# Performance work log

Hardware: AMD Instinct MI355X
Metric: run time of the kernel (lower is better)

The kernel has to match this reference:

```python
import jax, jax.numpy as jnp
import numpy as np

NT = 128
T = 262144


def setup_inputs() -> dict:
    key = jax.random.key(0)
    k1, k2, k3, k4, k5 = jax.random.split(key, 5)
    emit = jax.random.normal(k1, (T, NT), dtype=jnp.float32)
    y = jax.random.randint(k2, (T,), 0, NT, dtype=jnp.int64)
    trans = jax.random.normal(k3, (NT, NT), dtype=jnp.float32)
    strans = jax.random.normal(k4, (NT,), dtype=jnp.float32)
    etrans = jax.random.normal(k5, (NT,), dtype=jnp.float32)
    return {"emit": emit, "y": y, "trans": trans, "strans": strans, "etrans": etrans}


def _crf_nll(emit, y, trans, strans, etrans):
    Tlen = emit.shape[0]

    # forward algorithm (log partition) via scan over timesteps 1..T-1
    alpha0 = strans + emit[0]  # [nt]

    def step(alpha, e_t):
        # alpha_new[n] = logsumexp_p(alpha[p] + trans[p, n]) + emit_t[n]
        alpha_new = jax.nn.logsumexp(alpha[:, None] + trans, axis=0) + e_t
        return alpha_new, None

    alpha, _ = jax.lax.scan(step, alpha0, emit[1:])
    logZ = jax.nn.logsumexp(alpha + etrans)

    # gold score (faithful to original: emissions indexed by the *previous* tag)
    prev = y[:-1]
    nxt = y[1:]
    score = strans[y[0]]
    score = score + jnp.sum(trans[prev, nxt] + emit[jnp.arange(Tlen - 1), prev])
    score = score + etrans[y[-1]] + emit[-1, y[-1]]

    return logZ - score


def reference(emit, y, trans, strans, etrans):
    return _crf_nll(emit, y, trans, strans, etrans)
```

## Files before the change

### kernel.cpp

```cpp
#include <hip/hip_runtime.h>

typedef float f32x4 __attribute__((ext_vector_type(4)));

#define T_LEN   262144
#define NTAG    128
#define LCH     8
#define BURN    8
#define NSTEP   (LCH + BURN)
#define NCHUNK  (T_LEN / LCH)
#define NWAVE   (NCHUNK / 16)
#define NFWDB   (NWAVE / 4)
#define NSCOREB 256
#define NBLK    (NFWDB + NSCOREB)

__global__ __launch_bounds__(256, 1) void crf_all(
    const float* __restrict__ emit, const int* __restrict__ y,
    const float* __restrict__ trans, const float* __restrict__ strans,
    const float* __restrict__ etrans, double* __restrict__ ws,
    float* __restrict__ out)
{
  if (blockIdx.x < NFWDB) {
    const int w   = threadIdx.x >> 6;
    const int l   = threadIdx.x & 63;
    const int col = l & 15;
    const int grp = l >> 4;
    const int gw  = blockIdx.x * 4 + w;
    const int gc  = gw * 16 + col;

    long a[8][4];
#pragma unroll
    for (int rt = 0; rt < 8; ++rt) {
      const int outtag = 16 * rt + col;
#pragma unroll
      for (int kt = 0; kt < 4; ++kt) {
        float q[8];
#pragma unroll
        for (int j = 0; j < 8; ++j) {
          const int k = 32 * kt + 4 * grp + (j & 3) + 16 * (j >> 2);
          q[j] = __expf(trans[k * NTAG + outtag]);
        }
        unsigned lo = (unsigned)__builtin_amdgcn_cvt_pk_fp8_f32(q[0], q[1], 0, false);
        lo = (unsigned)__builtin_amdgcn_cvt_pk_fp8_f32(q[2], q[3], (int)lo, true);
        unsigned hi = (unsigned)__builtin_amdgcn_cvt_pk_fp8_f32(q[4], q[5], 0, false);
        hi = (unsigned)__builtin_amdgcn_cvt_pk_fp8_f32(q[6], q[7], (int)hi, true);
        a[rt][kt] = (long)(((unsigned long long)hi << 32) | lo);
      }
    }

    float acc = 0.f;
    long b[4];
    {
      float u[8][4];
      if (gc == 0) {
        float vm = -1e30f;
#pragma unroll
        for (int rt = 0; rt < 8; ++rt)
#pragma unroll
          for (int r = 0; r < 4; ++r) {
            const int tag = 16 * rt + 4 * grp + r;
            u[rt][r] = strans[tag] + emit[tag];
            vm = fmaxf(vm, u[rt][r]);
          }
        vm = fmaxf(vm, __shfl_xor(vm, 16, 64));
        vm = fmaxf(vm, __shfl_xor(vm, 32, 64));
        acc = vm;
#pragma unroll
        for (int rt = 0; rt < 8; ++rt)
#pragma unroll
          for (int r = 0; r < 4; ++r) u[rt][r] = __expf(u[rt][r] - vm);
      } else {
#pragma unroll
        for (int rt = 0; rt < 8; ++rt)
#pragma unroll
          for (int r = 0; r < 4; ++r) u[rt][r] = 1.0f;
      }
#pragma unroll
      for (int kt = 0; kt < 4; ++kt) {
        unsigned lo = (unsigned)__builtin_amdgcn_cvt_pk_fp8_f32(u[2*kt][0], u[2*kt][1], 0, false);
        lo = (unsigned)__builtin_amdgcn_cvt_pk_fp8_f32(u[2*kt][2], u[2*kt][3], (int)lo, true);
        unsigned hi = (unsigned)__builtin_amdgcn_cvt_pk_fp8_f32(u[2*kt+1][0], u[2*kt+1][1], 0, false);
        hi = (unsigned)__builtin_amdgcn_cvt_pk_fp8_f32(u[2*kt+1][2], u[2*kt+1][3], (int)hi, true);
        b[kt] = (long)(((unsigned long long)hi << 32) | lo);
      }
    }

    const int t0 = (gc == 0) ? 1 : (gc * LCH - BURN);
    float4 pf[8];
    {
      const float* ep = emit + ((size_t)t0 << 7) + 4 * grp;
#pragma unroll
      for (int rt = 0; rt < 8; ++rt) pf[rt] = *(const float4*)(ep + 16 * rt);
    }

#pragma unroll 1
    for (int s = 0; s < NSTEP; ++s) {
      f32x4 c[8];
#pragma unroll
      for (int rt = 0; rt < 8; ++rt) c[rt] = (f32x4){0.f, 0.f, 0.f, 0.f};
#pragma unroll
      for (int kt = 0; kt < 4; ++kt)
#pragma unroll
        for (int rt = 0; rt < 8; ++rt)
          c[rt] = __builtin_amdgcn_mfma_f32_16x16x32_fp8_fp8(a[rt][kt], b[kt], c[rt], 0, 0, 0);

      float vm = -1e30f;
#pragma unroll
      for (int rt = 0; rt < 8; ++rt) {
        c[rt][0] *= __expf(pf[rt].x);
        c[rt][1] *= __expf(pf[rt].y);
        c[rt][2] *= __expf(pf[rt].z);
        c[rt][3] *= __expf(pf[rt].w);
        vm = fmaxf(vm, fmaxf(fmaxf(c[rt][0], c[rt][1]), fmaxf(c[rt][2], c[rt][3])));
      }
      if (s < NSTEP - 1) {
        const float* ep = emit + ((size_t)(t0 + s + 1) << 7) + 4 * grp;
#pragma unroll
        for (int rt = 0; rt < 8; ++rt) pf[rt] = *(const float4*)(ep + 16 * rt);
      }

      vm = fmaxf(vm, __shfl_xor(vm, 16, 64));
      vm = fmaxf(vm, __shfl_xor(vm, 32, 64));
      const bool on = (gc == 0) ? (s <= LCH - 2) : (s >= BURN);
      if (on) acc += __logf(vm);
      const float rinv = __frcp_rn(vm);
#pragma unroll
      for (int kt = 0; kt < 4; ++kt) {
        const float s0 = c[2*kt][0] * rinv,   s1 = c[2*kt][1] * rinv;
        const float s2 = c[2*kt][2] * rinv,   s3 = c[2*kt][3] * rinv;
        const float s4 = c[2*kt+1][0] * rinv, s5 = c[2*kt+1][1] * rinv;
        const float s6 = c[2*kt+1][2] * rinv, s7 = c[2*kt+1][3] * rinv;
        unsigned lo = (unsigned)__builtin_amdgcn_cvt_pk_fp8_f32(s0, s1, 0, false);
        lo = (unsigned)__builtin_amdgcn_cvt_pk_fp8_f32(s2, s3, (int)lo, true);
        unsigned hi = (unsigned)__builtin_amdgcn_cvt_pk_fp8_f32(s4, s5, 0, false);
        hi = (unsigned)__builtin_amdgcn_cvt_pk_fp8_f32(s6, s7, (int)hi, true);
        b[kt] = (long)(((unsigned long long)hi << 32) | lo);
      }

      if (s == NSTEP - 1 && gc == NCHUNK - 1) {
        float lv = 0.f;
#pragma unroll
        for (int rt = 0; rt < 8; ++rt)
#pragma unroll
          for (int r = 0; r < 4; ++r)
            lv += (c[rt][r] * rinv) * __expf(etrans[16 * rt + 4 * grp + r]);
        lv += __shfl_xor(lv, 16, 64);
        lv += __shfl_xor(lv, 32, 64);
        if (l == 15) atomicAdd(&ws[2], (double)lv);
      }
    }

    float av = (grp == 0) ? acc : 0.f;
#pragma unroll
    for (int off = 1; off < 64; off <<= 1) av += __shfl_xor(av, off, 64);
    if (l == 0) atomicAdd(&ws[0], (double)av);
  } else {
    __shared__ float sred[4];
    int idx0 = (blockIdx.x - NFWDB) * 256 + threadIdx.x;
    float v = 0.f;
    for (int t = idx0; t < T_LEN - 1; t += NSCOREB * 256) {
      int yt = y[t], yn = y[t + 1];
      v += trans[yt * NTAG + yn] + emit[(size_t)t * NTAG + yt];
    }
    if (idx0 == 0) {
      int yl = y[T_LEN - 1];
      v += strans[y[0]] + etrans[yl] + emit[(size_t)(T_LEN - 1) * NTAG + yl];
    }
#pragma unroll
    for (int off = 1; off < 64; off <<= 1) v += __shfl_xor(v, off, 64);
    if ((threadIdx.x & 63) == 0) sred[threadIdx.x >> 6] = v;
    __syncthreads();
    if (threadIdx.x == 0)
      atomicAdd(&ws[1], (double)(sred[0] + sred[1] + sred[2] + sred[3]));
  }

  __syncthreads();
  if (threadIdx.x == 0) {
    __threadfence();
    unsigned t = atomicAdd((unsigned*)&ws[3], 1u);
    if (t == NBLK - 1) {
      double d0 = atomicAdd(&ws[0], 0.0);
      double d1 = atomicAdd(&ws[1], 0.0);
      double d2 = atomicAdd(&ws[2], 0.0);
      out[0] = (float)(d0 + log(d2) - d1);
    }
  }
}

extern "C" void kernel_launch(void* const* d_in, const int* in_sizes, int n_in,
                              void* d_out, int out_size, void* d_ws, size_t ws_size,
                              hipStream_t stream)
{
  const float* emit   = (const float*)d_in[0];
  const int*   y      = (const int*)d_in[1];
  const float* trans  = (const float*)d_in[2];
  const float* strans = (const float*)d_in[3];
  const float* etrans = (const float*)d_in[4];
  float*  out = (float*)d_out;
  double* ws  = (double*)d_ws;

  hipMemsetAsync(ws, 0, 4 * sizeof(double), stream);
  crf_all<<<dim3(NBLK), dim3(256), 0, stream>>>(
      emit, y, trans, strans, etrans, ws, out);
}
```

Measured before the change: 92.53 us.

## Split CRF kernel, precompute fp8 transition matrix, renormalize every four steps

New measurement: 82.38 us. -11.0%, faster.

```diff
diff --git a/kernel.cpp b/kernel.cpp
--- a/kernel.cpp
+++ b/kernel.cpp
@@ -6,35 +6,26 @@
 #define NTAG    128
 #define LCH     8
 #define BURN    8
-#define NSTEP   (LCH + BURN)
+#define NSTEP   16
 #define NCHUNK  (T_LEN / LCH)
 #define NWAVE   (NCHUNK / 16)
 #define NFWDB   (NWAVE / 4)
 #define NSCOREB 256
-#define NBLK    (NFWDB + NSCOREB)
-
-__global__ __launch_bounds__(256, 1) void crf_all(
-    const float* __restrict__ emit, const int* __restrict__ y,
-    const float* __restrict__ trans, const float* __restrict__ strans,
-    const float* __restrict__ etrans, double* __restrict__ ws,
-    float* __restrict__ out)
-{
-  if (blockIdx.x < NFWDB) {
-    const int w   = threadIdx.x >> 6;
-    const int l   = threadIdx.x & 63;
-    const int col = l & 15;
-    const int grp = l >> 4;
-    const int gw  = blockIdx.x * 4 + w;
-    const int gc  = gw * 16 + col;
-
-    long a[8][4];
-#pragma unroll
-    for (int rt = 0; rt < 8; ++rt) {
-      const int outtag = 16 * rt + col;
-#pragma unroll
-      for (int kt = 0; kt < 4; ++kt) {
+#define C9      6.23832462503951f
+#define K63LN2  43.66827237527655f
+#define K72LN2  49.90659700060892f
+
+__global__ void crf_setup(const float* __restrict__ trans, uint4* __restrict__ q4)
+{
+  const int l = threadIdx.x;
+  const int col = l & 15, grp = l >> 4;
+  for (int rt = 0; rt < 8; ++rt) {
+    const int outtag = 16 * rt + col;
+    for (int kp = 0; kp < 2; ++kp) {
+      unsigned r[4];
+      for (int h = 0; h < 2; ++h) {
+        const int kt = kp * 2 + h;
         float q[8];
-#pragma unroll
         for (int j = 0; j < 8; ++j) {
           const int k = 32 * kt + 4 * grp + (j & 3) + 16 * (j >> 2);
           q[j] = __expf(trans[k * NTAG + outtag]);
@@ -43,147 +34,204 @@
         lo = (unsigned)__builtin_amdgcn_cvt_pk_fp8_f32(q[2], q[3], (int)lo, true);
         unsigned hi = (unsigned)__builtin_amdgcn_cvt_pk_fp8_f32(q[4], q[5], 0, false);
         hi = (unsigned)__builtin_amdgcn_cvt_pk_fp8_f32(q[6], q[7], (int)hi, true);
-        a[rt][kt] = (long)(((unsigned long long)hi << 32) | lo);
+        r[h * 2] = lo; r[h * 2 + 1] = hi;
       }
-    }
-
-    float acc = 0.f;
-    long b[4];
-    {
-      float u[8][4];
-      if (gc == 0) {
-        float vm = -1e30f;
+      q4[(rt * 2 + kp) * 64 + l] = make_uint4(r[0], r[1], r[2], r[3]);
+    }
+  }
+}
+
+__global__ __launch_bounds__(256, 2) void crf_fwd(
+    const float* __restrict__ emit, const float* __restrict__ strans,
+    const float* __restrict__ etrans, const uint4* __restrict__ q4,
+    double* __restrict__ ws)
+{
+  const int w_id = threadIdx.x >> 6;
+  const int l    = threadIdx.x & 63;
+  const int col  = l & 15;
+  const int grp  = l >> 4;
+  const int gw   = blockIdx.x * 4 + w_id;
+  const int gc   = gw * 16 + col;
+
+  long a[8][4];
+#pragma unroll
+  for (int rt = 0; rt < 8; ++rt)
+#pragma unroll
+    for (int kp = 0; kp < 2; ++kp) {
+      uint4 v = q4[(rt * 2 + kp) * 64 + l];
+      a[rt][2 * kp]     = (long)(((unsigned long long)v.y << 32) | v.x);
+      a[rt][2 * kp + 1] = (long)(((unsigned long long)v.w << 32) | v.z);
+    }
+
+  float m0 = 0.f;
+  long b[4];
+  {
+    float u[8][4];
+    if (gw == 0) {
+      float vm = -1e30f;
+#pragma unroll
+      for (int rt = 0; rt < 8; ++rt)
+#pragma unroll
+        for (int r = 0; r < 4; ++r) {
+          const int tag = 16 * rt + 4 * grp + r;
+          u[rt][r] = (col == 0) ? (strans[tag] + emit[tag]) : 0.f;
+          vm = fmaxf(vm, u[rt][r]);
+        }
+      vm = fmaxf(vm, __shfl_xor(vm, 16, 64));
+      vm = fmaxf(vm, __shfl_xor(vm, 32, 64));
+      m0 = vm;
+#pragma unroll
+      for (int rt = 0; rt < 8; ++rt)
+#pragma unroll
+        for (int r = 0; r < 4; ++r)
+          u[rt][r] = (col == 0) ? __expf(u[rt][r] - vm) : 1.0f;
+    } else {
+#pragma unroll
+      for (int rt = 0; rt < 8; ++rt)
+#pragma unroll
+        for (int r = 0; r < 4; ++r) u[rt][r] = 1.0f;
+    }
+#pragma unroll
+    for (int kt = 0; kt < 4; ++kt) {
+      unsigned lo = (unsigned)__builtin_amdgcn_cvt_pk_fp8_f32(u[2*kt][0], u[2*kt][1], 0, false);
+      lo = (unsigned)__builtin_amdgcn_cvt_pk_fp8_f32(u[2*kt][2], u[2*kt][3], (int)lo, true);
+      unsigned hi = (unsigned)__builtin_amdgcn_cvt_pk_fp8_f32(u[2*kt+1][0], u[2*kt+1][1], 0, false);
+      hi = (unsigned)__builtin_amdgcn_cvt_pk_fp8_f32(u[2*kt+1][2], u[2*kt+1][3], (int)hi, true);
+      b[kt] = (long)(((unsigned long long)hi << 32) | lo);
+    }
+  }
+
+  const int t0 = (gc == 0) ? 1 : (gc * LCH - BURN);
+  float4 pf[2][8];
+  {
+    const float* e0 = emit + ((size_t)t0 << 7) + 4 * grp;
+    const float* e1 = emit + ((size_t)(t0 + 1) << 7) + 4 * grp;
+#pragma unroll
+    for (int rt = 0; rt < 8; ++rt) {
+      pf[0][rt] = *(const float4*)(e0 + 16 * rt);
+      pf[1][rt] = *(const float4*)(e1 + 16 * rt);
+    }
+  }
+
+  float acc = 0.f;
+
+#pragma unroll
+  for (int s = 0; s < NSTEP; ++s) {
+    float e[8][4];
+#pragma unroll
+    for (int rt = 0; rt < 8; ++rt) {
+      e[rt][0] = __expf(pf[s & 1][rt].x - C9);
+      e[rt][1] = __expf(pf[s & 1][rt].y - C9);
+      e[rt][2] = __expf(pf[s & 1][rt].z - C9);
+      e[rt][3] = __expf(pf[s & 1][rt].w - C9);
+    }
+    if (s < NSTEP - 2) {
+      const float* ep = emit + ((size_t)(t0 + s + 2) << 7) + 4 * grp;
+#pragma unroll
+      for (int rt = 0; rt < 8; ++rt) pf[s & 1][rt] = *(const float4*)(ep + 16 * rt);
+    }
+
+    f32x4 c[8];
+#pragma unroll
+    for (int rt = 0; rt < 8; ++rt) c[rt] = (f32x4){0.f, 0.f, 0.f, 0.f};
+#pragma unroll
+    for (int kt = 0; kt < 4; ++kt)
+#pragma unroll
+      for (int rt = 0; rt < 8; ++rt)
+        c[rt] = __builtin_amdgcn_mfma_f32_16x16x32_fp8_fp8(a[rt][kt], b[kt], c[rt], 0, 0, 0);
+
+    float w[8][4];
+#pragma unroll
+    for (int rt = 0; rt < 8; ++rt)
+#pragma unroll
+      for (int r = 0; r < 4; ++r) w[rt][r] = c[rt][r] * e[rt][r];
+
+    if ((s & 3) == 3) {
+      float vm = w[0][0];
+#pragma unroll
+      for (int rt = 0; rt < 8; ++rt)
+#pragma unroll
+        for (int r = 0; r < 4; ++r) vm = fmaxf(vm, w[rt][r]);
+      vm = fmaxf(vm, __shfl_xor(vm, 16, 64));
+      vm = fmaxf(vm, __shfl_xor(vm, 32, 64));
+      const float lv = __logf(vm);
+      if (s == 3)  acc += (gc == 0) ? lv : 0.f;
+      if (s == 11) acc += (gc != 0) ? lv : 0.f;
+      if (s == 15) acc += (gc != 0) ? lv : 0.f;
+      const float rinv = __builtin_amdgcn_rcpf(vm);
+#pragma unroll
+      for (int rt = 0; rt < 8; ++rt)
+#pragma unroll
+        for (int r = 0; r < 4; ++r) w[rt][r] *= rinv;
+
+      if (s == NSTEP - 1 && gw == NWAVE - 1) {
+        float lse = 0.f;
 #pragma unroll
         for (int rt = 0; rt < 8; ++rt)
 #pragma unroll
-          for (int r = 0; r < 4; ++r) {
-            const int tag = 16 * rt + 4 * grp + r;
-            u[rt][r] = strans[tag] + emit[tag];
-            vm = fmaxf(vm, u[rt][r]);
-          }
+          for (int r = 0; r < 4; ++r)
+            lse += w[rt][r] * __expf(etrans[16 * rt + 4 * grp + r]);
+        lse += __shfl_xor(lse, 16, 64);
+        lse += __shfl_xor(lse, 32, 64);
+        if (l == 15) atomicAdd(&ws[2], (double)lse);
+      }
+    }
+    if (s == 6) {
+      if (gw == 0) {
+        float vm = w[0][0];
+#pragma unroll
+        for (int rt = 0; rt < 8; ++rt)
+#pragma unroll
+          for (int r = 0; r < 4; ++r) vm = fmaxf(vm, w[rt][r]);
         vm = fmaxf(vm, __shfl_xor(vm, 16, 64));
         vm = fmaxf(vm, __shfl_xor(vm, 32, 64));
-        acc = vm;
-#pragma unroll
-        for (int rt = 0; rt < 8; ++rt)
-#pragma unroll
-          for (int r = 0; r < 4; ++r) u[rt][r] = __expf(u[rt][r] - vm);
-      } else {
-#pragma unroll
-        for (int rt = 0; rt < 8; ++rt)
-#pragma unroll
-          for (int r = 0; r < 4; ++r) u[rt][r] = 1.0f;
+        acc += (gc == 0) ? __logf(vm) : 0.f;
       }
-#pragma unroll
-      for (int kt = 0; kt < 4; ++kt) {
-        unsigned lo = (unsigned)__builtin_amdgcn_cvt_pk_fp8_f32(u[2*kt][0], u[2*kt][1], 0, false);
-        lo = (unsigned)__builtin_amdgcn_cvt_pk_fp8_f32(u[2*kt][2], u[2*kt][3], (int)lo, true);
-        unsigned hi = (unsigned)__builtin_amdgcn_cvt_pk_fp8_f32(u[2*kt+1][0], u[2*kt+1][1], 0, false);
-        hi = (unsigned)__builtin_amdgcn_cvt_pk_fp8_f32(u[2*kt+1][2], u[2*kt+1][3], (int)hi, true);
-        b[kt] = (long)(((unsigned long long)hi << 32) | lo);
-      }
-    }
-
-    const int t0 = (gc == 0) ? 1 : (gc * LCH - BURN);
-    float4 pf[8];
-    {
-      const float* ep = emit + ((size_t)t0 << 7) + 4 * grp;
-#pragma unroll
-      for (int rt = 0; rt < 8; ++rt) pf[rt] = *(const float4*)(ep + 16 * rt);
-    }
-
-#pragma unroll 1
-    for (int s = 0; s < NSTEP; ++s) {
-      f32x4 c[8];
-#pragma unroll
-      for (int rt = 0; rt < 8; ++rt) c[rt] = (f32x4){0.f, 0.f, 0.f, 0.f};
-#pragma unroll
-      for (int kt = 0; kt < 4; ++kt)
-#pragma unroll
-        for (int rt = 0; rt < 8; ++rt)
-          c[rt] = __builtin_amdgcn_mfma_f32_16x16x32_fp8_fp8(a[rt][kt], b[kt], c[rt], 0, 0, 0);
-
-      float vm = -1e30f;
-#pragma unroll
-      for (int rt = 0; rt < 8; ++rt) {
-        c[rt][0] *= __expf(pf[rt].x);
-        c[rt][1] *= __expf(pf[rt].y);
-        c[rt][2] *= __expf(pf[rt].z);
-        c[rt][3] *= __expf(pf[rt].w);
-        vm = fmaxf(vm, fmaxf(fmaxf(c[rt][0], c[rt][1]), fmaxf(c[rt][2], c[rt][3])));
-      }
-      if (s < NSTEP - 1) {
-        const float* ep = emit + ((size_t)(t0 + s + 1) << 7) + 4 * grp;
-#pragma unroll
-        for (int rt = 0; rt < 8; ++rt) pf[rt] = *(const float4*)(ep + 16 * rt);
-      }
-
-      vm = fmaxf(vm, __shfl_xor(vm, 16, 64));
-      vm = fmaxf(vm, __shfl_xor(vm, 32, 64));
-      const bool on = (gc == 0) ? (s <= LCH - 2) : (s >= BURN);
-      if (on) acc += __logf(vm);
-      const float rinv = __frcp_rn(vm);
-#pragma unroll
-      for (int kt = 0; kt < 4; ++kt) {
-        const float s0 = c[2*kt][0] * rinv,   s1 = c[2*kt][1] * rinv;
-        const float s2 = c[2*kt][2] * rinv,   s3 = c[2*kt][3] * rinv;
-        const float s4 = c[2*kt+1][0] * rinv, s5 = c[2*kt+1][1] * rinv;
-        const float s6 = c[2*kt+1][2] * rinv, s7 = c[2*kt+1][3] * rinv;
-        unsigned lo = (unsigned)__builtin_amdgcn_cvt_pk_fp8_f32(s0, s1, 0, false);
-        lo = (unsigned)__builtin_amdgcn_cvt_pk_fp8_f32(s2, s3, (int)lo, true);
-        unsigned hi = (unsigned)__builtin_amdgcn_cvt_pk_fp8_f32(s4, s5, 0, false);
-        hi = (unsigned)__builtin_amdgcn_cvt_pk_fp8_f32(s6, s7, (int)hi, true);
-        b[kt] = (long)(((unsigned long long)hi << 32) | lo);
-      }
-
-      if (s == NSTEP - 1 && gc == NCHUNK - 1) {
-        float lv = 0.f;
-#pragma unroll
-        for (int rt = 0; rt < 8; ++rt)
-#pragma unroll
-          for (int r = 0; r < 4; ++r)
-            lv += (c[rt][r] * rinv) * __expf(etrans[16 * rt + 4 * grp + r]);
-        lv += __shfl_xor(lv, 16, 64);
-        lv += __shfl_xor(lv, 32, 64);
-        if (l == 15) atomicAdd(&ws[2], (double)lv);
-      }
-    }
-
-    float av = (grp == 0) ? acc : 0.f;
-#pragma unroll
-    for (int off = 1; off < 64; off <<= 1) av += __shfl_xor(av, off, 64);
-    if (l == 0) atomicAdd(&ws[0], (double)av);
-  } else {
-    __shared__ float sred[4];
-    int idx0 = (blockIdx.x - NFWDB) * 256 + threadIdx.x;
-    float v = 0.f;
-    for (int t = idx0; t < T_LEN - 1; t += NSCOREB * 256) {
-      int yt = y[t], yn = y[t + 1];
-      v += trans[yt * NTAG + yn] + emit[(size_t)t * NTAG + yt];
-    }
-    if (idx0 == 0) {
-      int yl = y[T_LEN - 1];
-      v += strans[y[0]] + etrans[yl] + emit[(size_t)(T_LEN - 1) * NTAG + yl];
-    }
-#pragma unroll
-    for (int off = 1; off < 64; off <<= 1) v += __shfl_xor(v, off, 64);
-    if ((threadIdx.x & 63) == 0) sred[threadIdx.x >> 6] = v;
-    __syncthreads();
-    if (threadIdx.x == 0)
-      atomicAdd(&ws[1], (double)(sred[0] + sred[1] + sred[2] + sred[3]));
-  }
-
+    }
+
+#pragma unroll
+    for (int kt = 0; kt < 4; ++kt) {
+      unsigned lo = (unsigned)__builtin_amdgcn_cvt_pk_fp8_f32(w[2*kt][0], w[2*kt][1], 0, false);
+      lo = (unsigned)__builtin_amdgcn_cvt_pk_fp8_f32(w[2*kt][2], w[2*kt][3], (int)lo, true);
+      unsigned hi = (unsigned)__builtin_amdgcn_cvt_pk_fp8_f32(w[2*kt+1][0], w[2*kt+1][1], 0, false);
+      hi = (unsigned)__builtin_amdgcn_cvt_pk_fp8_f32(w[2*kt+1][2], w[2*kt+1][3], (int)hi, true);
+      b[kt] = (long)(((unsigned long long)hi << 32) | lo);
+    }
+  }
+
+  const float accf = acc + ((gc == 0) ? (m0 + K63LN2) : K72LN2);
+  float av = (grp == 0) ? accf : 0.f;
+#pragma unroll
+  for (int off = 1; off < 64; off <<= 1) av += __shfl_xor(av, off, 64);
+  if (l == 0) atomicAdd(&ws[0], (double)av);
+}
+
+__global__ void crf_score(const float* __restrict__ emit, const int* __restrict__ y,
+                          const float* __restrict__ trans, const float* __restrict__ strans,
+                          const float* __restrict__ etrans, double* __restrict__ ws)
+{
+  __shared__ float sred[4];
+  int idx0 = blockIdx.x * 256 + threadIdx.x;
+  float v = 0.f;
+  for (int t = idx0; t < T_LEN - 1; t += NSCOREB * 256) {
+    int yt = y[t], yn = y[t + 1];
+    v += trans[yt * NTAG + yn] + emit[(size_t)t * NTAG + yt];
+  }
+  if (idx0 == 0) {
+    int yl = y[T_LEN - 1];
+    v += strans[y[0]] + etrans[yl] + emit[(size_t)(T_LEN - 1) * NTAG + yl];
+  }
+#pragma unroll
+  for (int off = 1; off < 64; off <<= 1) v += __shfl_xor(v, off, 64);
+  if ((threadIdx.x & 63) == 0) sred[threadIdx.x >> 6] = v;
   __syncthreads();
-  if (threadIdx.x == 0) {
-    __threadfence();
-    unsigned t = atomicAdd((unsigned*)&ws[3], 1u);
-    if (t == NBLK - 1) {
-      double d0 = atomicAdd(&ws[0], 0.0);
-      double d1 = atomicAdd(&ws[1], 0.0);
-      double d2 = atomicAdd(&ws[2], 0.0);
-      out[0] = (float)(d0 + log(d2) - d1);
-    }
-  }
+  if (threadIdx.x == 0)
+    atomicAdd(&ws[1], (double)(sred[0] + sred[1] + sred[2] + sred[3]));
+}
+
+__global__ void crf_final(const double* __restrict__ ws, float* __restrict__ out)
+{
+  out[0] = (float)(ws[0] + log(ws[2]) - ws[1]);
 }
 
 extern "C" void kernel_launch(void* const* d_in, const int* in_sizes, int n_in,
@@ -197,8 +245,11 @@
   const float* etrans = (const float*)d_in[4];
   float*  out = (float*)d_out;
   double* ws  = (double*)d_ws;
+  uint4*  q4  = (uint4*)((char*)d_ws + 64);
 
   hipMemsetAsync(ws, 0, 4 * sizeof(double), stream);
-  crf_all<<<dim3(NBLK), dim3(256), 0, stream>>>(
-      emit, y, trans, strans, etrans, ws, out);
-}
+  crf_setup<<<dim3(1), dim3(64), 0, stream>>>(trans, q4);
+  crf_score<<<dim3(NSCOREB), dim3(256), 0, stream>>>(emit, y, trans, strans, etrans, ws);
+  crf_fwd<<<dim3(NFWDB), dim3(256), 0, stream>>>(emit, strans, etrans, q4, ws);
+  crf_final<<<dim3(1), dim3(1), 0, stream>>>(ws, out);
+}
```
